# Optimization experiments

Measured on AMD Instinct MI355X. Metric: run time of the kernel, lower is better.

The kernel has to match this reference:

```python
import math
import jax, jax.numpy as jnp
import numpy as np

D_MODEL = 2048
N_HEADS = 16


def setup_inputs() -> dict:
    key = jax.random.key(0)
    ks = jax.random.split(key, 5)
    d = D_MODEL
    x = jax.random.normal(ks[0], (256, 64, d), dtype=jnp.float32)
    # nn.Linear(d, 3d): weight [3d, d], bias [3d]
    W_qkv = jax.random.normal(ks[1], (3 * d, d), dtype=jnp.float32) * (1.0 / math.sqrt(d))
    b_qkv = jnp.zeros((3 * d,), dtype=jnp.float32)
    W_out = jax.random.normal(ks[2], (d, d), dtype=jnp.float32) * (1.0 / math.sqrt(d))
    b_out = jnp.zeros((d,), dtype=jnp.float32)
    return {"x": x, "W_qkv": W_qkv, "b_qkv": b_qkv, "W_out": W_out, "b_out": b_out}


def reference(x, W_qkv, b_qkv, W_out, b_out):
    B, S, d = x.shape
    H = N_HEADS
    hd = d // H
    qkv = jnp.einsum('bsd,ed->bse', x, W_qkv) + b_qkv  # [B,S,3d]
    q, k, v = jnp.split(qkv, 3, axis=2)
    # [B,S,H,hd] -> [B,H,S,hd]
    q = q.reshape(B, S, H, hd).transpose(0, 2, 1, 3)
    k = k.reshape(B, S, H, hd).transpose(0, 2, 1, 3)
    v = v.reshape(B, S, H, hd).transpose(0, 2, 1, 3)
    attn = jnp.einsum('bhqd,bhkd->bhqk', q, k) / math.sqrt(d)  # NOTE: scaled by sqrt(d_model)
    causal = jnp.tril(jnp.ones((S, S), dtype=bool))  # [S,S]
    attn = jnp.where(causal[None, None], attn, -jnp.inf)
    # NOTE: faithful to source, softmax over dim=-2 (query axis)
    attn = jax.nn.softmax(attn, axis=-2)
    out = jnp.einsum('bhqk,bhkd->bhqd', attn, v)  # [B,H,S,hd]
    out = out.transpose(0, 2, 1, 3).reshape(B, S, d)
    return jnp.einsum('bsd,ed->bse', out, W_out) + b_out
```

## Files before the change

### kernel.cpp

```cpp
#include <hip/hip_runtime.h>
#include <hip/hip_fp16.h>

typedef _Float16 f16x8 __attribute__((ext_vector_type(8)));
typedef _Float16 f16x2 __attribute__((ext_vector_type(2)));
typedef float f32x4 __attribute__((ext_vector_type(4)));
typedef short s16x8 __attribute__((ext_vector_type(8)));

typedef __attribute__((address_space(1))) void gvoid;
typedef __attribute__((address_space(3))) void lvoid;

#define GLD_LDS16(g, l) __builtin_amdgcn_global_load_lds((gvoid*)(g), (lvoid*)(l), 16, 0, 0)
#define BAR() __builtin_amdgcn_s_barrier()

__global__ __launch_bounds__(256) void cvt_f32_f16(
    const float* __restrict__ src, _Float16* __restrict__ dst, int n8)
{
    const int i = blockIdx.x * 256 + threadIdx.x;
    if (i >= n8) return;
    const float4* s = (const float4*)src;
    const float4 a = s[2 * i], b = s[2 * i + 1];
    f16x8 o;
    o[0] = (_Float16)a.x; o[1] = (_Float16)a.y; o[2] = (_Float16)a.z; o[3] = (_Float16)a.w;
    o[4] = (_Float16)b.x; o[5] = (_Float16)b.y; o[6] = (_Float16)b.z; o[7] = (_Float16)b.w;
    *(f16x8*)(dst + (size_t)i * 8) = o;
}

template <typename OutT>
__global__ __launch_bounds__(512, 1) void gemm_bt_bias(
    const _Float16* __restrict__ A, int lda,
    const _Float16* __restrict__ B,
    const float* __restrict__ bias,
    OutT* __restrict__ C, int ldc,
    int K, int nbx)
{
    __shared__ alignas(16) _Float16 smem[65536];

    const int tid = threadIdx.x;
    const int lane = tid & 63, wv = tid >> 6;
    const int nwg = gridDim.x;
    int bid = blockIdx.x;
    if ((nwg & 7) == 0) bid = (bid & 7) * (nwg >> 3) + (bid >> 3);
    const int m0 = (bid / nbx) * 256, n0 = (bid % nbx) * 256;
    const int wm = wv >> 2, wn = wv & 3;
    const int l15 = lane & 15, q4 = lane >> 4, l7 = lane & 7;
    const int nk = K >> 6;

    const int rl = tid >> 3;
    const int cl = (tid & 7) ^ (rl & 7);
    const _Float16* gp00 = A + (size_t)(m0 + rl) * lda + cl * 8;
    const _Float16* gp01 = A + (size_t)(m0 + 64 + rl) * lda + cl * 8;
    const _Float16* gp10 = A + (size_t)(m0 + 128 + rl) * lda + cl * 8;
    const _Float16* gp11 = A + (size_t)(m0 + 192 + rl) * lda + cl * 8;
    const _Float16* gp20 = B + (size_t)(n0 + rl) * (size_t)K + cl * 8;
    const _Float16* gp21 = B + (size_t)(n0 + 64 + rl) * (size_t)K + cl * 8;
    const _Float16* gp30 = B + (size_t)(n0 + 128 + rl) * (size_t)K + cl * 8;
    const _Float16* gp31 = B + (size_t)(n0 + 192 + rl) * (size_t)K + cl * 8;

    f32x4 acc[8][4];
#pragma unroll
    for (int i = 0; i < 8; ++i)
#pragma unroll
        for (int j = 0; j < 4; ++j)
            acc[i][j] = (f32x4){0.f, 0.f, 0.f, 0.f};

    f16x8 fa[4][2], fb0[2][2], fb1[2][2];

#define STAGE(J, tile_) do {                                                  \
    const int dd_ = (tile_) & 1;                                              \
    _Float16* lb_ = &smem[dd_ * 32768 + ((J) >> 1) * 16384 +                  \
                          ((J) & 1) * 8192 + wv * 512];                       \
    const size_t ko_ = (size_t)(tile_) * 64;                                  \
    GLD_LDS16(gp##J##0 + ko_, lb_);                                           \
    GLD_LDS16(gp##J##1 + ko_, lb_ + 4096);                                    \
} while (0)

#define RD_A(d_, mq_) do {                                                    \
    const _Float16* ba_ = &smem[(d_) * 32768];                                \
    _Pragma("unroll")                                                         \
    for (int fi = 0; fi < 4; ++fi) {                                          \
        const int r_ = wm * 128 + (mq_) * 64 + fi * 16 + l15;                 \
        fa[fi][0] = *(const f16x8*)(ba_ + r_ * 64 + ((q4 ^ l7) * 8));         \
        fa[fi][1] = *(const f16x8*)(ba_ + r_ * 64 + (((4 + q4) ^ l7) * 8));   \
    }                                                                         \
} while (0)

#define RD_B(d_, nq_, fbv) do {                                               \
    const _Float16* bb_ = &smem[(d_) * 32768 + 16384];                        \
    _Pragma("unroll")                                                         \
    for (int fj = 0; fj < 2; ++fj) {                                          \
        const int r_ = wn * 64 + (nq_) * 32 + fj * 16 + l15;                  \
        fbv[fj][0] = *(const f16x8*)(bb_ + r_ * 64 + ((q4 ^ l7) * 8));        \
        fbv[fj][1] = *(const f16x8*)(bb_ + r_ * 64 + (((4 + q4) ^ l7) * 8));  \
    }                                                                         \
} while (0)

#define MM(mq_, nq_, fbv) do {                                                \
    __builtin_amdgcn_s_setprio(1);                                            \
    _Pragma("unroll")                                                         \
    for (int ks = 0; ks < 2; ++ks)                                            \
    _Pragma("unroll")                                                         \
    for (int fi = 0; fi < 4; ++fi)                                            \
    _Pragma("unroll")                                                         \
    for (int fj = 0; fj < 2; ++fj)                                            \
        acc[(mq_) * 4 + fi][(nq_) * 2 + fj] =                                 \
            __builtin_amdgcn_mfma_f32_16x16x32_f16(                           \
                fa[fi][ks], fbv[fj][ks],                                      \
                acc[(mq_) * 4 + fi][(nq_) * 2 + fj], 0, 0, 0);                \
    __builtin_amdgcn_s_setprio(0);                                            \
} while (0)

#define GTILE(d_, S1, S2, S3, S4, VMN) do {                                   \
    RD_A(d_, 0); RD_B(d_, 0, fb0);                                           \
    S1;                                                                       \
    BAR(); MM(0, 0, fb0); BAR();                                              \
    RD_B(d_, 1, fb1);                                                         \
    S2;                                                                       \
    BAR(); MM(0, 1, fb1); BAR();                                              \
    RD_A(d_, 1);                                                              \
    S3;                                                                       \
    BAR(); MM(1, 1, fb1); BAR();                                              \
    S4;                                                                       \
    BAR(); MM(1, 0, fb0);                                                     \
    asm volatile("s_waitcnt vmcnt(" #VMN ")" ::: "memory");                   \
    BAR();                                                                    \
} while (0)

    STAGE(0, 0); STAGE(1, 0); STAGE(2, 0); STAGE(3, 0);
    if (nk > 1) {
        STAGE(0, 1);
        asm volatile("s_waitcnt vmcnt(2)" ::: "memory");
    } else {
        asm volatile("s_waitcnt vmcnt(0)" ::: "memory");
    }
    BAR();

    for (int kt = 0; kt < nk - 2; ++kt) {
        const int d = kt & 1;
        GTILE(d, STAGE(1, kt + 1), STAGE(2, kt + 1), STAGE(3, kt + 1),
              STAGE(0, kt + 2), 2);
    }
    if (nk >= 2) {
        GTILE((nk - 2) & 1, STAGE(1, nk - 1), STAGE(2, nk - 1),
              STAGE(3, nk - 1), (void)0, 0);
    }
    {
        const int d = (nk - 1) & 1;
        RD_A(d, 0); RD_B(d, 0, fb0);
        MM(0, 0, fb0);
        RD_B(d, 1, fb1);
        MM(0, 1, fb1);
        RD_A(d, 1);
        MM(1, 1, fb1);
        MM(1, 0, fb0);
    }

#undef GTILE
#undef MM
#undef RD_B
#undef RD_A
#undef STAGE

#pragma unroll
    for (int nj = 0; nj < 4; ++nj) {
        const int col = n0 + wn * 64 + nj * 16 + l15;
        const float bs = bias[col];
#pragma unroll
        for (int mi = 0; mi < 8; ++mi) {
            const int row = m0 + wm * 128 + mi * 16 + q4 * 4;
#pragma unroll
            for (int i = 0; i < 4; ++i)
                C[(size_t)(row + i) * ldc + col] = (OutT)(acc[mi][nj][i] + bs);
        }
    }
}

__global__ __launch_bounds__(256) void attn_fused(_Float16* __restrict__ qkv)
{
    constexpr float SCALE = 0.022097086912079608f;
    __shared__ alignas(16) char smem[51968];
    __shared__ float sRed[256];
    _Float16* sQ = (_Float16*)smem;
    _Float16* sK = (_Float16*)(smem + 17408);
    _Float16* sV = (_Float16*)(smem + 34816);
    float* sSt = (float*)smem;
    _Float16* sP = (_Float16*)(smem + 17408);

    const int t = threadIdx.x;
    const int bh = blockIdx.x;
    const int b = bh >> 4, h = bh & 15;
    const int ld = 6144;
    const _Float16* Qg = qkv + (size_t)b * 64 * ld + h * 128;
    const _Float16* Kg = Qg + 2048;
    const _Float16* Vg = Qg + 4096;
    _Float16* Og = qkv + (size_t)b * 64 * ld + h * 128;

    for (int i = t; i < 1024; i += 256) {
        const int r = i >> 4, c = (i & 15) * 8;
        *(s16x8*)(sQ + r * 136 + c) = *(const s16x8*)(Qg + (size_t)r * ld + c);
        *(s16x8*)(sK + r * 136 + c) = *(const s16x8*)(Kg + (size_t)r * ld + c);
        const f16x8 vv = *(const f16x8*)(Vg + (size_t)r * ld + c);
#pragma unroll
        for (int p = 0; p < 4; ++p) {
            f16x2 w2; w2[0] = vv[2 * p]; w2[1] = vv[2 * p + 1];
            *(f16x2*)(sV + r * 134 + c + 2 * p) = w2;
        }
    }
    __syncthreads();

    const int lane = t & 63, w = t >> 6;
    const int l15 = lane & 15, q4 = lane >> 4;
    const f32x4 fz = {0.f, 0.f, 0.f, 0.f};

    f32x4 sc[4];
#pragma unroll
    for (int nt = 0; nt < 4; ++nt) sc[nt] = fz;
#pragma unroll
    for (int kk = 0; kk < 128; kk += 32) {
        const f16x8 aq = *(const f16x8*)(sQ + (w * 16 + l15) * 136 + kk + q4 * 8);
#pragma unroll
        for (int nt = 0; nt < 4; ++nt) {
            const f16x8 bk = *(const f16x8*)(sK + (nt * 16 + l15) * 136 + kk + q4 * 8);
            sc[nt] = __builtin_amdgcn_mfma_f32_16x16x32_f16(aq, bk, sc[nt], 0, 0, 0);
        }
    }
    __syncthreads();

#pragma unroll
    for (int nt = 0; nt < 4; ++nt)
#pragma unroll
        for (int i = 0; i < 4; ++i)
            sSt[(nt * 16 + l15) * 65 + (w * 16 + q4 * 4 + i)] = sc[nt][i] * SCALE;
    __syncthreads();

    {
        const int k = t >> 2, j = t & 3;
        const int qlo = max(k, j * 16), qhi = min(64, j * 16 + 16);
        float mx = -3.0e38f;
        for (int q = qlo; q < qhi; ++q) mx = fmaxf(mx, sSt[k * 65 + q]);
        sRed[t] = mx;
        __syncthreads();
        mx = fmaxf(fmaxf(sRed[k * 4 + 0], sRed[k * 4 + 1]),
                   fmaxf(sRed[k * 4 + 2], sRed[k * 4 + 3]));
        float sum = 0.f;
        for (int q = qlo; q < qhi; ++q) {
            const float e = __expf(sSt[k * 65 + q] - mx);
            sSt[k * 65 + q] = e;
            sum += e;
        }
        sRed[t] = sum;
        __syncthreads();
        const float inv = 1.f / (sRed[k * 4 + 0] + sRed[k * 4 + 1] +
                                 sRed[k * 4 + 2] + sRed[k * 4 + 3]);
        for (int q = j * 16; q < j * 16 + 16; ++q) {
            const float p = (q >= k) ? sSt[k * 65 + q] * inv : 0.f;
            sP[q * 72 + k] = (_Float16)p;
        }
    }
    __syncthreads();

    f32x4 oa[8];
#pragma unroll
    for (int nt = 0; nt < 8; ++nt) oa[nt] = fz;
#pragma unroll
    for (int kk = 0; kk < 64; kk += 32) {
        const f16x8 ap = *(const f16x8*)(sP + (w * 16 + l15) * 72 + kk + q4 * 8);
#pragma unroll
        for (int nt = 0; nt < 8; ++nt) {
            f16x8 bv;
#pragma unroll
            for (int j = 0; j < 8; ++j)
                bv[j] = sV[(kk + q4 * 8 + j) * 134 + nt * 16 + l15];
            oa[nt] = __builtin_amdgcn_mfma_f32_16x16x32_f16(ap, bv, oa[nt], 0, 0, 0);
        }
    }
#pragma unroll
    for (int nt = 0; nt < 8; ++nt)
#pragma unroll
        for (int i = 0; i < 4; ++i)
            Og[(size_t)(w * 16 + q4 * 4 + i) * ld + nt * 16 + l15] =
                (_Float16)(oa[nt][i]);
}

extern "C" void kernel_launch(void* const* d_in, const int* in_sizes, int n_in,
                              void* d_out, int out_size, void* d_ws, size_t ws_size,
                              hipStream_t stream) {
    const float* x     = (const float*)d_in[0];
    const float* W_qkv = (const float*)d_in[1];
    const float* b_qkv = (const float*)d_in[2];
    const float* W_out = (const float*)d_in[3];
    const float* b_out = (const float*)d_in[4];
    float* out = (float*)d_out;

    char* ws = (char*)d_ws;
    _Float16* qkv = (_Float16*)ws;
    _Float16* xh  = (_Float16*)(ws + 201326592);
    _Float16* wqh = (_Float16*)(ws + 268435456);
    _Float16* woh = wqh;

    cvt_f32_f16<<<dim3(33554432 / 2048), 256, 0, stream>>>(x, xh, 33554432 / 8);
    cvt_f32_f16<<<dim3(12582912 / 2048), 256, 0, stream>>>(W_qkv, wqh, 12582912 / 8);
    gemm_bt_bias<_Float16><<<dim3(1536), 512, 0, stream>>>(
        xh, 2048, wqh, b_qkv, qkv, 6144, 2048, 24);
    cvt_f32_f16<<<dim3(4194304 / 2048), 256, 0, stream>>>(W_out, woh, 4194304 / 8);
    attn_fused<<<dim3(4096), 256, 0, stream>>>(qkv);
    gemm_bt_bias<float><<<dim3(512), 512, 0, stream>>>(
        qkv, 6144, woh, b_out, out, 2048, 2048, 8);
}
```

Before: 842.1 us.

## Do register-resident column softmax and store V transposed with swizzle in attention

The score MFMA now runs with keys as rows, so each wave holds whole key rows in registers. The column softmax over the query axis then uses cross-lane shuffles instead of a shared-memory staging pass with several barriers. V is stored transposed with an XOR-style swizzle, so PV operands load as single 16-byte vectors instead of eight scalar LDS reads. An occupancy hint of three blocks per CU is added. Attention is likely a small share of the total time next to the two GEMMs, so the overall effect may be limited.

```diff
diff --git a/kernel.cpp b/kernel.cpp
--- a/kernel.cpp
+++ b/kernel.cpp
@@ -2,7 +2,7 @@
 #include <hip/hip_fp16.h>
 
 typedef _Float16 f16x8 __attribute__((ext_vector_type(8)));
-typedef _Float16 f16x2 __attribute__((ext_vector_type(2)));
+typedef _Float16 f16x4 __attribute__((ext_vector_type(4)));
 typedef float f32x4 __attribute__((ext_vector_type(4)));
 typedef short s16x8 __attribute__((ext_vector_type(8)));
 
@@ -174,16 +174,14 @@
     }
 }
 
-__global__ __launch_bounds__(256) void attn_fused(_Float16* __restrict__ qkv)
+__global__ __launch_bounds__(256, 3) void attn_fused(_Float16* __restrict__ qkv)
 {
     constexpr float SCALE = 0.022097086912079608f;
-    __shared__ alignas(16) char smem[51968];
-    __shared__ float sRed[256];
-    _Float16* sQ = (_Float16*)smem;
-    _Float16* sK = (_Float16*)(smem + 17408);
-    _Float16* sV = (_Float16*)(smem + 34816);
-    float* sSt = (float*)smem;
-    _Float16* sP = (_Float16*)(smem + 17408);
+    __shared__ alignas(16) char smem[53248];
+    _Float16* sQ  = (_Float16*)smem;
+    _Float16* sK  = (_Float16*)(smem + 17408);
+    _Float16* sVT = (_Float16*)(smem + 34816);
+    _Float16* sP  = (_Float16*)smem;
 
     const int t = threadIdx.x;
     const int bh = blockIdx.x;
@@ -194,85 +192,100 @@
     const _Float16* Vg = Qg + 4096;
     _Float16* Og = qkv + (size_t)b * 64 * ld + h * 128;
 
-    for (int i = t; i < 1024; i += 256) {
+    const int lane = t & 63, w = t >> 6;
+    const int l15 = lane & 15, q4 = lane >> 4;
+
+#pragma unroll
+    for (int j = 0; j < 4; ++j) {
+        const int i = t + j * 256;
         const int r = i >> 4, c = (i & 15) * 8;
         *(s16x8*)(sQ + r * 136 + c) = *(const s16x8*)(Qg + (size_t)r * ld + c);
         *(s16x8*)(sK + r * 136 + c) = *(const s16x8*)(Kg + (size_t)r * ld + c);
         const f16x8 vv = *(const f16x8*)(Vg + (size_t)r * ld + c);
-#pragma unroll
-        for (int p = 0; p < 4; ++p) {
-            f16x2 w2; w2[0] = vv[2 * p]; w2[1] = vv[2 * p + 1];
-            *(f16x2*)(sV + r * 134 + c + 2 * p) = w2;
+        const int cp = ((r >> 3) + (c >> 3)) & 7;
+#pragma unroll
+        for (int p = 0; p < 8; ++p)
+            sVT[(c + p) * 72 + cp * 8 + (r & 7)] = vv[p];
+    }
+    __syncthreads();
+
+    f32x4 sc[4];
+#pragma unroll
+    for (int nt = 0; nt < 4; ++nt) sc[nt] = (f32x4){0.f, 0.f, 0.f, 0.f};
+#pragma unroll
+    for (int kk = 0; kk < 4; ++kk) {
+        const f16x8 ak = *(const f16x8*)(sK + (w * 16 + l15) * 136 + kk * 32 + q4 * 8);
+#pragma unroll
+        for (int nt = 0; nt < 4; ++nt) {
+            const f16x8 bq = *(const f16x8*)(sQ + (nt * 16 + l15) * 136 + kk * 32 + q4 * 8);
+            sc[nt] = __builtin_amdgcn_mfma_f32_16x16x32_f16(ak, bq, sc[nt], 0, 0, 0);
         }
     }
+
+    const int key0 = w * 16 + q4 * 4;
+#pragma unroll
+    for (int nt = 0; nt < 4; ++nt) {
+        const int q = nt * 16 + l15;
+#pragma unroll
+        for (int i = 0; i < 4; ++i)
+            sc[nt][i] = (q >= key0 + i) ? sc[nt][i] * SCALE : -3.0e38f;
+    }
+
+    float mx[4], sm[4];
+#pragma unroll
+    for (int i = 0; i < 4; ++i)
+        mx[i] = fmaxf(fmaxf(sc[0][i], sc[1][i]), fmaxf(sc[2][i], sc[3][i]));
+#pragma unroll
+    for (int m = 1; m <= 8; m <<= 1)
+#pragma unroll
+        for (int i = 0; i < 4; ++i)
+            mx[i] = fmaxf(mx[i], __shfl_xor(mx[i], m, 64));
+#pragma unroll
+    for (int i = 0; i < 4; ++i) sm[i] = 0.f;
+#pragma unroll
+    for (int nt = 0; nt < 4; ++nt)
+#pragma unroll
+        for (int i = 0; i < 4; ++i) {
+            const float e = __expf(sc[nt][i] - mx[i]);
+            sc[nt][i] = e;
+            sm[i] += e;
+        }
+#pragma unroll
+    for (int m = 1; m <= 8; m <<= 1)
+#pragma unroll
+        for (int i = 0; i < 4; ++i)
+            sm[i] += __shfl_xor(sm[i], m, 64);
+    float inv[4];
+#pragma unroll
+    for (int i = 0; i < 4; ++i) inv[i] = 1.0f / sm[i];
+
     __syncthreads();
 
-    const int lane = t & 63, w = t >> 6;
-    const int l15 = lane & 15, q4 = lane >> 4;
-    const f32x4 fz = {0.f, 0.f, 0.f, 0.f};
-
-    f32x4 sc[4];
-#pragma unroll
-    for (int nt = 0; nt < 4; ++nt) sc[nt] = fz;
-#pragma unroll
-    for (int kk = 0; kk < 128; kk += 32) {
-        const f16x8 aq = *(const f16x8*)(sQ + (w * 16 + l15) * 136 + kk + q4 * 8);
-#pragma unroll
-        for (int nt = 0; nt < 4; ++nt) {
-            const f16x8 bk = *(const f16x8*)(sK + (nt * 16 + l15) * 136 + kk + q4 * 8);
-            sc[nt] = __builtin_amdgcn_mfma_f32_16x16x32_f16(aq, bk, sc[nt], 0, 0, 0);
-        }
+#pragma unroll
+    for (int nt = 0; nt < 4; ++nt) {
+        f16x4 pk;
+#pragma unroll
+        for (int i = 0; i < 4; ++i)
+            pk[i] = (_Float16)(sc[nt][i] * inv[i]);
+        *(f16x4*)(sP + (nt * 16 + l15) * 72 + w * 16 + q4 * 4) = pk;
     }
     __syncthreads();
 
-#pragma unroll
-    for (int nt = 0; nt < 4; ++nt)
-#pragma unroll
-        for (int i = 0; i < 4; ++i)
-            sSt[(nt * 16 + l15) * 65 + (w * 16 + q4 * 4 + i)] = sc[nt][i] * SCALE;
-    __syncthreads();
-
-    {
-        const int k = t >> 2, j = t & 3;
-        const int qlo = max(k, j * 16), qhi = min(64, j * 16 + 16);
-        float mx = -3.0e38f;
-        for (int q = qlo; q < qhi; ++q) mx = fmaxf(mx, sSt[k * 65 + q]);
-        sRed[t] = mx;
-        __syncthreads();
-        mx = fmaxf(fmaxf(sRed[k * 4 + 0], sRed[k * 4 + 1]),
-                   fmaxf(sRed[k * 4 + 2], sRed[k * 4 + 3]));
-        float sum = 0.f;
-        for (int q = qlo; q < qhi; ++q) {
-            const float e = __expf(sSt[k * 65 + q] - mx);
-            sSt[k * 65 + q] = e;
-            sum += e;
-        }
-        sRed[t] = sum;
-        __syncthreads();
-        const float inv = 1.f / (sRed[k * 4 + 0] + sRed[k * 4 + 1] +
-                                 sRed[k * 4 + 2] + sRed[k * 4 + 3]);
-        for (int q = j * 16; q < j * 16 + 16; ++q) {
-            const float p = (q >= k) ? sSt[k * 65 + q] * inv : 0.f;
-            sP[q * 72 + k] = (_Float16)p;
-        }
-    }
-    __syncthreads();
-
     f32x4 oa[8];
 #pragma unroll
-    for (int nt = 0; nt < 8; ++nt) oa[nt] = fz;
-#pragma unroll
-    for (int kk = 0; kk < 64; kk += 32) {
-        const f16x8 ap = *(const f16x8*)(sP + (w * 16 + l15) * 72 + kk + q4 * 8);
+    for (int nt = 0; nt < 8; ++nt) oa[nt] = (f32x4){0.f, 0.f, 0.f, 0.f};
+#pragma unroll
+    for (int ks = 0; ks < 2; ++ks) {
+        const int cc = ks * 4 + q4;
+        const f16x8 ap = *(const f16x8*)(sP + (w * 16 + l15) * 72 + cc * 8);
 #pragma unroll
         for (int nt = 0; nt < 8; ++nt) {
-            f16x8 bv;
-#pragma unroll
-            for (int j = 0; j < 8; ++j)
-                bv[j] = sV[(kk + q4 * 8 + j) * 134 + nt * 16 + l15];
+            const int dd = nt * 16 + l15;
+            const f16x8 bv = *(const f16x8*)(sVT + dd * 72 + ((cc + (dd >> 3)) & 7) * 8);
             oa[nt] = __builtin_amdgcn_mfma_f32_16x16x32_f16(ap, bv, oa[nt], 0, 0, 0);
         }
     }
+
 #pragma unroll
     for (int nt = 0; nt < 8; ++nt)
 #pragma unroll
```

New measurement: 799.4 us. 5.1% less time.
